# Performance work log

Hardware: AMD Instinct MI355X
Metric: run time of the kernel (lower is better)

The kernel has to match this reference:

```python
import jax, jax.numpy as jnp
import numpy as np

N_HEADS = 16
D_HEAD = 64
D_MODEL = 1024
WINDOW = 256
B, T = 4, 2048


def rotate_half(x):
    x1, x2 = jnp.split(x, 2, axis=-1)
    return jnp.concatenate([-x2, x1], axis=-1)


def apply_rope(x, cos, sin):
    return x * cos + rotate_half(x) * sin


def setup_inputs() -> dict:
    key = jax.random.key(0)
    ks = jax.random.split(key, 5)
    x = jax.random.normal(ks[0], (B, T, D_MODEL), dtype=jnp.float32)
    cos = jax.random.normal(ks[1], (1, T, 1, D_HEAD), dtype=jnp.float32)
    sin = jax.random.normal(ks[2], (1, T, 1, D_HEAD), dtype=jnp.float32)
    qkv_w = jax.random.normal(ks[3], (3 * D_MODEL, D_MODEL), dtype=jnp.float32) * (D_MODEL ** -0.5)
    out_w = jax.random.normal(ks[4], (D_MODEL, D_MODEL), dtype=jnp.float32) * (D_MODEL ** -0.5)
    return {"x": x, "cos": cos, "sin": sin, "qkv_w": qkv_w, "out_w": out_w}


def reference(x, cos, sin, qkv_w, out_w):
    Bc, Tc, C = x.shape
    # QKV projection (bias-free Linear: y = x @ W^T)
    qkv = jnp.einsum('btc,fc->btf', x, qkv_w)
    q, k, v = jnp.split(qkv, 3, axis=-1)
    # [B, H, T, d]
    def to_heads(t):
        return t.reshape(Bc, Tc, N_HEADS, D_HEAD).transpose(0, 2, 1, 3)
    q, k, v = to_heads(q), to_heads(k), to_heads(v)
    # RoPE: cos/sin [1, T, 1, d] -> [1, 1, T, d] broadcasting over heads
    cos_t = cos[:, :Tc].transpose(0, 2, 1, 3)
    sin_t = sin[:, :Tc].transpose(0, 2, 1, 3)
    q = apply_rope(q, cos_t, sin_t)
    k = apply_rope(k, cos_t, sin_t)
    # banded causal mask: allow j <= i and j >= i - (window-1)
    i = jnp.arange(Tc)[:, None]
    j = jnp.arange(Tc)[None, :]
    allowed = (j <= i) & (j >= i - (WINDOW - 1))  # [T, T]
    scale = 1.0 / jnp.sqrt(jnp.asarray(D_HEAD, dtype=q.dtype))
    scores = jnp.einsum('bhqd,bhkd->bhqk', q, k) * scale
    scores = jnp.where(allowed[None, None], scores, jnp.finfo(scores.dtype).min)
    attn = jax.nn.softmax(scores, axis=-1)
    out = jnp.einsum('bhqk,bhkd->bhqd', attn, v)
    out = out.transpose(0, 2, 1, 3).reshape(Bc, Tc, C)
    return jnp.einsum('btc,oc->bto', out, out_w)
```

## Files before the change

kernel.cpp:

```cpp
#include <hip/hip_runtime.h>

typedef __bf16 bf16_t;
typedef __bf16 bf16x8 __attribute__((ext_vector_type(8)));
typedef __bf16 bf16x4 __attribute__((ext_vector_type(4)));
typedef float f32x4 __attribute__((ext_vector_type(4)));

#define GLOAD_LDS16(gptr, lptr)                                                              \
  __builtin_amdgcn_global_load_lds((const __attribute__((address_space(1))) void*)(gptr),    \
                                   (__attribute__((address_space(3))) void*)(lptr), 16, 0, 0)

__device__ __forceinline__ f32x4 f32x4_zero() {
  f32x4 v; v[0] = 0.f; v[1] = 0.f; v[2] = 0.f; v[3] = 0.f; return v;
}

__device__ __forceinline__ int kxr(int r) { return (r & 7) ^ (((r >> 3) & 3) << 1); }

__global__ void cast3_kernel(const float* __restrict__ a, const float* __restrict__ b,
                             const float* __restrict__ c, bf16_t* __restrict__ oa,
                             bf16_t* __restrict__ ob, bf16_t* __restrict__ oc) {
  int i = blockIdx.x * blockDim.x + threadIdx.x;
  const float* src; bf16_t* dst; int j;
  if (i < 2097152) { src = a; dst = oa; j = i; }
  else if (i < 2883584) { src = b; dst = ob; j = i - 2097152; }
  else { src = c; dst = oc; j = i - 2883584; }
  float4 v = ((const float4*)src)[j];
  bf16x4 o;
  o[0] = (bf16_t)v.x; o[1] = (bf16_t)v.y; o[2] = (bf16_t)v.z; o[3] = (bf16_t)v.w;
  ((bf16x4*)dst)[j] = o;
}

#define GT_AELE 16384
#define GT_BELE 8192
#define GT_TILE (GT_AELE + GT_BELE)

__device__ __forceinline__ void gt_stage(const bf16_t* __restrict__ A,
                                         const bf16_t* __restrict__ B, bf16_t* buf,
                                         int bm, int bn, int t, int K, int tid) {
#pragma unroll
  for (int i = 0; i < 4; i++) {
    int gi = tid + i * 512;
    int row = gi >> 3, g = gi & 7;
    const bf16_t* src = A + (size_t)(bm * 256 + row) * K + t * 64 + ((g ^ (row & 7)) << 3);
    GLOAD_LDS16(src, buf + gi * 8);
  }
#pragma unroll
  for (int i = 0; i < 2; i++) {
    int gi = tid + i * 512;
    int row = gi >> 3, g = gi & 7;
    const bf16_t* src = B + (size_t)(bn * 128 + row) * K + t * 64 + ((g ^ (row & 7)) << 3);
    GLOAD_LDS16(src, buf + GT_AELE + gi * 8);
  }
}

template <int MODE>
__global__ __launch_bounds__(512, 1) void gemm_bt_kernel(
    const bf16_t* __restrict__ A, const bf16_t* __restrict__ B, float* __restrict__ C,
    bf16_t* __restrict__ oq, bf16_t* __restrict__ ok_, bf16_t* __restrict__ ov,
    const float* __restrict__ cosp, const float* __restrict__ sinp,
    int M, int N, int K) {
  __shared__ bf16_t lds[3 * GT_TILE];

  const int tid = threadIdx.x;
  const int lane = tid & 63;
  const int wid = tid >> 6;
  const int wr = wid >> 1;
  const int wc = wid & 1;
  const int l16 = lane & 15;
  const int qd = lane >> 4;
  const int bm = blockIdx.x, bn = blockIdx.y;

  f32x4 acc[4][4];
#pragma unroll
  for (int m = 0; m < 4; m++)
#pragma unroll
    for (int n = 0; n < 4; n++) acc[m][n] = f32x4_zero();

  const int NT = K >> 6;

  gt_stage(A, B, lds, bm, bn, 0, K, tid);
  gt_stage(A, B, lds + GT_TILE, bm, bn, 1, K, tid);
  asm volatile("s_waitcnt vmcnt(6)" ::: "memory");
  __builtin_amdgcn_s_barrier();
  __builtin_amdgcn_sched_barrier(0);

  int s = 0;
  for (int j = 0; j < NT; ++j) {
    if (j + 2 < NT) {
      int s2 = s + 2; if (s2 >= 3) s2 -= 3;
      gt_stage(A, B, lds + s2 * GT_TILE, bm, bn, j + 2, K, tid);
    }

    const bf16_t* bufc = lds + s * GT_TILE;
    bf16x8 af[4][2], bf[4][2];
#pragma unroll
    for (int m = 0; m < 4; m++)
#pragma unroll
      for (int kk = 0; kk < 2; kk++) {
        int row = wr * 64 + m * 16 + l16;
        af[m][kk] = *(const bf16x8*)&bufc[row * 64 + (((kk * 4 + qd) ^ (row & 7)) << 3)];
      }
#pragma unroll
    for (int n = 0; n < 4; n++)
#pragma unroll
      for (int kk = 0; kk < 2; kk++) {
        int row = wc * 64 + n * 16 + l16;
        bf[n][kk] = *(const bf16x8*)&bufc[GT_AELE + row * 64 + (((kk * 4 + qd) ^ (row & 7)) << 3)];
      }

    __builtin_amdgcn_s_setprio(1);
#pragma unroll
    for (int m = 0; m < 4; m++)
#pragma unroll
      for (int n = 0; n < 4; n++)
#pragma unroll
        for (int kk = 0; kk < 2; kk++)
          acc[m][n] = __builtin_amdgcn_mfma_f32_16x16x32_bf16(af[m][kk], bf[n][kk], acc[m][n], 0, 0, 0);
    __builtin_amdgcn_s_setprio(0);

    if (j + 2 < NT) {
      asm volatile("s_waitcnt vmcnt(6)" ::: "memory");
    } else {
      asm volatile("s_waitcnt vmcnt(0)" ::: "memory");
    }
    __builtin_amdgcn_s_barrier();
    __builtin_amdgcn_sched_barrier(0);
    s = (s == 2) ? 0 : s + 1;
  }

  if (MODE == 0) {
#pragma unroll
    for (int m = 0; m < 4; m++)
#pragma unroll
      for (int n = 0; n < 4; n++)
#pragma unroll
        for (int r = 0; r < 4; r++) {
          int row = bm * 256 + wr * 64 + m * 16 + qd * 4 + r;
          int col = bn * 128 + wc * 64 + n * 16 + l16;
          C[(size_t)row * N + col] = acc[m][n][r];
        }
  } else {
    const int colbase = bn * 128 + wc * 64;
    const int part = colbase >> 10;
    const int h = (colbase & 1023) >> 6;
    bf16_t* dst = (part == 0) ? oq : (part == 1) ? ok_ : ov;
    if (part == 2) {
#pragma unroll
      for (int m = 0; m < 4; m++)
#pragma unroll
        for (int r = 0; r < 4; r++) {
          int row = bm * 256 + wr * 64 + m * 16 + qd * 4 + r;
          int b = row >> 11, t = row & 2047;
          size_t basei = (((size_t)(b * 16 + h)) * 2048 + t) * 64;
#pragma unroll
          for (int n = 0; n < 4; n++)
            dst[basei + n * 16 + l16] = (bf16_t)acc[m][n][r];
        }
    } else {
      const float qsc = (part == 0) ? 0.18033688011112042f : 1.0f;
#pragma unroll
      for (int m = 0; m < 4; m++)
#pragma unroll
        for (int r = 0; r < 4; r++) {
          int row = bm * 256 + wr * 64 + m * 16 + qd * 4 + r;
          int b = row >> 11, t = row & 2047;
          size_t basei = (((size_t)(b * 16 + h)) * 2048 + t) * 64;
#pragma unroll
          for (int nb = 0; nb < 2; nb++) {
            int d = nb * 16 + l16;
            float xl = acc[m][nb][r];
            float xh = acc[m][nb + 2][r];
            float cl = cosp[t * 64 + d], ch = cosp[t * 64 + d + 32];
            float sl = sinp[t * 64 + d], sh = sinp[t * 64 + d + 32];
            dst[basei + d]      = (bf16_t)((xl * cl - xh * sl) * qsc);
            dst[basei + d + 32] = (bf16_t)((xh * ch + xl * sh) * qsc);
          }
        }
    }
  }
}

__global__ __launch_bounds__(256) void attn_kernel(
    const bf16_t* __restrict__ qh, const bf16_t* __restrict__ kh,
    const bf16_t* __restrict__ vh, bf16_t* __restrict__ ao) {
  __shared__ bf16_t qs[64 * 64];
  __shared__ bf16_t ks[64 * 64];
  __shared__ bf16_t vs[64 * 64];
  __shared__ bf16_t vswz[8 * 64 * 8];
  __shared__ bf16_t ps[4][16 * 64];

  const int tid = threadIdx.x;
  const int lane = tid & 63;
  const int wid = tid >> 6;
  const int l16 = lane & 15;
  const int qd = lane >> 4;

  const int bh = blockIdx.x;
  const int i0 = blockIdx.y * 64;
  const int b = bh >> 4, h = bh & 15;

  auto swz4 = [](int f) { int r = f >> 3; return r * 8 + ((f & 7) ^ (r & 7)); };
  const int r0 = tid >> 3, q0 = tid & 7;

  {
    const uint4* src = (const uint4*)(qh + ((size_t)bh * 2048 + i0) * 64);
    uint4* dst = (uint4*)qs;
    dst[swz4(tid)] = src[tid];
    dst[swz4(tid + 256)] = src[tid + 256];
  }

  bf16x8 bones;
#pragma unroll
  for (int e = 0; e < 8; e++) bones[e] = (bf16_t)1.0f;

  float l_i[4] = {0.f, 0.f, 0.f, 0.f};
  f32x4 oacc[4];
#pragma unroll
  for (int nb = 0; nb < 4; nb++) oacc[nb] = f32x4_zero();

  const int c1 = i0 >> 6;
  const int c0 = (c1 >= 4) ? (c1 - 4) : 0;

  for (int c = c0; c <= c1; c++) {
    const int j0 = c * 64;
    __syncthreads();
    {
      const uint4* ksrc = (const uint4*)(kh + ((size_t)bh * 2048 + j0) * 64);
      const uint4* vsrc = (const uint4*)(vh + ((size_t)bh * 2048 + j0) * 64);
      uint4* kdst = (uint4*)ks; uint4* vdst = (uint4*)vs;
      kdst[swz4(tid)] = ksrc[tid]; kdst[swz4(tid + 256)] = ksrc[tid + 256];
      vdst[r0 * 8 + (q0 ^ kxr(r0))] = vsrc[tid];
      vdst[(r0 + 32) * 8 + (q0 ^ kxr(r0 + 32))] = vsrc[tid + 256];
    }
    __syncthreads();

    f32x4 sacc[4];
#pragma unroll
    for (int nb = 0; nb < 4; nb++) sacc[nb] = f32x4_zero();
#pragma unroll
    for (int kk = 0; kk < 2; kk++) {
      bf16x8 afr = *(const bf16x8*)&qs[(wid * 16 + l16) * 64 + (((kk * 4 + qd) ^ (l16 & 7)) * 8)];
#pragma unroll
      for (int nb = 0; nb < 4; nb++) {
        bf16x8 bfr = *(const bf16x8*)&ks[(nb * 16 + l16) * 64 + (((kk * 4 + qd) ^ (l16 & 7)) * 8)];
        sacc[nb] = __builtin_amdgcn_mfma_f32_16x16x32_bf16(afr, bfr, sacc[nb], 0, 0, 0);
      }
    }

#pragma unroll
    for (int p2 = 0; p2 < 2; p2++) {
      int combo = p2 * 4 + wid;
      int jbase = (combo >> 2) * 32 + (lane >> 4) * 8;
      int dcol = (combo & 3) * 16 + (lane & 15);
      int bb = dcol >> 3, dlo = dcol & 7;
      bf16x8 v8;
#pragma unroll
      for (int e = 0; e < 8; e++) {
        int row = jbase + e;
        v8[e] = vs[row * 64 + ((bb ^ kxr(row)) * 8) + dlo];
      }
      *(bf16x8*)&vswz[(combo * 64 + lane) * 8] = v8;
    }

#pragma unroll
    for (int r = 0; r < 4; r++) {
      const int i = i0 + wid * 16 + qd * 4 + r;
      const int prow = qd * 4 + r;
#pragma unroll
      for (int nb = 0; nb < 4; nb++) {
        const int j = j0 + nb * 16 + l16;
        bool valid = (j <= i) && (j + 256 > i);
        float p = valid ? exp2f(sacc[nb][r]) : 0.f;
        ps[wid][prow * 64 + (((nb * 2 + (l16 >> 3)) ^ (prow & 7)) * 8) + (l16 & 7)] = (bf16_t)p;
      }
    }

    __syncthreads();

    f32x4 lacc = f32x4_zero();
#pragma unroll
    for (int kk = 0; kk < 2; kk++) {
      bf16x8 afr = *(const bf16x8*)&ps[wid][l16 * 64 + (((kk * 4 + qd) ^ (l16 & 7)) * 8)];
      lacc = __builtin_amdgcn_mfma_f32_16x16x32_bf16(afr, bones, lacc, 0, 0, 0);
#pragma unroll
      for (int nb = 0; nb < 4; nb++) {
        bf16x8 bfr = *(const bf16x8*)&vswz[((kk * 4 + nb) * 64 + lane) * 8];
        oacc[nb] = __builtin_amdgcn_mfma_f32_16x16x32_bf16(afr, bfr, oacc[nb], 0, 0, 0);
      }
    }
#pragma unroll
    for (int r = 0; r < 4; r++) l_i[r] += lacc[r];
  }

#pragma unroll
  for (int nb = 0; nb < 4; nb++) {
#pragma unroll
    for (int r = 0; r < 4; r++) {
      int t = i0 + wid * 16 + qd * 4 + r;
      ao[((size_t)(b * 2048 + t)) * 1024 + h * 64 + nb * 16 + l16] =
          (bf16_t)(oacc[nb][r] / l_i[r]);
    }
  }
}

extern "C" void kernel_launch(void* const* d_in, const int* in_sizes, int n_in,
                              void* d_out, int out_size, void* d_ws, size_t ws_size,
                              hipStream_t stream) {
  const float* x    = (const float*)d_in[0];
  const float* cosp = (const float*)d_in[1];
  const float* sinp = (const float*)d_in[2];
  const float* qkvw = (const float*)d_in[3];
  const float* outw = (const float*)d_in[4];
  float* out = (float*)d_out;

  char* ws = (char*)d_ws;
  bf16_t* xb  = (bf16_t*)(ws + 0);
  bf16_t* qwb = (bf16_t*)(ws + 16777216);
  bf16_t* owb = (bf16_t*)(ws + 23068672);
  bf16_t* qhp = (bf16_t*)(ws + 25165824);
  bf16_t* khp = (bf16_t*)(ws + 41943040);
  bf16_t* vhp = (bf16_t*)(ws + 58720256);
  bf16_t* aop = (bf16_t*)(ws + 75497472);

  cast3_kernel<<<12288, 256, 0, stream>>>(x, qkvw, outw, xb, qwb, owb);

  gemm_bt_kernel<1><<<dim3(32, 24), 512, 0, stream>>>(xb, qwb, nullptr, qhp, khp, vhp,
                                                      cosp, sinp, 8192, 3072, 1024);
  attn_kernel<<<dim3(64, 32), 256, 0, stream>>>(qhp, khp, vhp, aop);
  gemm_bt_kernel<0><<<dim3(32, 8), 512, 0, stream>>>(aop, owb, out, nullptr, nullptr, nullptr,
                                                     nullptr, nullptr, 8192, 1024, 1024);
}
```

Before: 219.0 us.

## Store V transposed from QKV GEMM epilogue and drop in-kernel V transpose

The QKV GEMM epilogue now writes V in a [B,H,d,T] transposed layout, staging each warp's tile through LDS so the global stores are 16-byte vectors. The attention kernel then loads V^T straight into a swizzled LDS tile that the PV MFMA can read directly. This removes the per-chunk scalar LDS gather into vswz and replaces one __syncthreads with a local lgkmcnt wait, since each warp reads only its own P rows. The risks are reusing the GEMM's LDS buffer in the epilogue and the uncoalesced 2048-stride rows of V^T loads.

```diff
diff --git a/kernel.cpp b/kernel.cpp
--- a/kernel.cpp
+++ b/kernel.cpp
@@ -12,8 +12,6 @@
 __device__ __forceinline__ f32x4 f32x4_zero() {
   f32x4 v; v[0] = 0.f; v[1] = 0.f; v[2] = 0.f; v[3] = 0.f; return v;
 }
-
-__device__ __forceinline__ int kxr(int r) { return (r & 7) ^ (((r >> 3) & 3) << 1); }
 
 __global__ void cast3_kernel(const float* __restrict__ a, const float* __restrict__ b,
                              const float* __restrict__ c, bf16_t* __restrict__ oa,
@@ -142,20 +140,35 @@
     const int colbase = bn * 128 + wc * 64;
     const int part = colbase >> 10;
     const int h = (colbase & 1023) >> 6;
-    bf16_t* dst = (part == 0) ? oq : (part == 1) ? ok_ : ov;
     if (part == 2) {
+      bf16_t* lw = lds + wid * 4096;
 #pragma unroll
       for (int m = 0; m < 4; m++)
 #pragma unroll
-        for (int r = 0; r < 4; r++) {
-          int row = bm * 256 + wr * 64 + m * 16 + qd * 4 + r;
-          int b = row >> 11, t = row & 2047;
-          size_t basei = (((size_t)(b * 16 + h)) * 2048 + t) * 64;
-#pragma unroll
-          for (int n = 0; n < 4; n++)
-            dst[basei + n * 16 + l16] = (bf16_t)acc[m][n][r];
+        for (int n = 0; n < 4; n++) {
+          int d = n * 16 + l16;
+          int gr = (m * 2 + (qd >> 1)) ^ (d & 7);
+          bf16x4 w;
+          w[0] = (bf16_t)acc[m][n][0];
+          w[1] = (bf16_t)acc[m][n][1];
+          w[2] = (bf16_t)acc[m][n][2];
+          w[3] = (bf16_t)acc[m][n][3];
+          *(bf16x4*)&lw[d * 64 + gr * 8 + (qd & 1) * 4] = w;
         }
+      asm volatile("s_waitcnt lgkmcnt(0)" ::: "memory");
+      __builtin_amdgcn_sched_barrier(0);
+      const int rowbase = bm * 256 + wr * 64;
+      const int bb = rowbase >> 11, tb = rowbase & 2047;
+      bf16_t* vbase = ov + ((size_t)(bb * 16 + h) * 64) * 2048 + tb;
+#pragma unroll
+      for (int it = 0; it < 8; it++) {
+        int d = it * 8 + (lane >> 3);
+        int g = lane & 7;
+        *(bf16x8*)&vbase[(size_t)d * 2048 + g * 8] =
+            *(const bf16x8*)&lw[d * 64 + ((g ^ (d & 7)) << 3)];
+      }
     } else {
+      bf16_t* dst = (part == 0) ? oq : ok_;
       const float qsc = (part == 0) ? 0.18033688011112042f : 1.0f;
 #pragma unroll
       for (int m = 0; m < 4; m++)
@@ -181,11 +194,10 @@
 
 __global__ __launch_bounds__(256) void attn_kernel(
     const bf16_t* __restrict__ qh, const bf16_t* __restrict__ kh,
-    const bf16_t* __restrict__ vh, bf16_t* __restrict__ ao) {
+    const bf16_t* __restrict__ vt, bf16_t* __restrict__ ao) {
   __shared__ bf16_t qs[64 * 64];
   __shared__ bf16_t ks[64 * 64];
-  __shared__ bf16_t vs[64 * 64];
-  __shared__ bf16_t vswz[8 * 64 * 8];
+  __shared__ bf16_t vts[64 * 64];
   __shared__ bf16_t ps[4][16 * 64];
 
   const int tid = threadIdx.x;
@@ -199,7 +211,6 @@
   const int b = bh >> 4, h = bh & 15;
 
   auto swz4 = [](int f) { int r = f >> 3; return r * 8 + ((f & 7) ^ (r & 7)); };
-  const int r0 = tid >> 3, q0 = tid & 7;
 
   {
     const uint4* src = (const uint4*)(qh + ((size_t)bh * 2048 + i0) * 64);
@@ -225,11 +236,16 @@
     __syncthreads();
     {
       const uint4* ksrc = (const uint4*)(kh + ((size_t)bh * 2048 + j0) * 64);
-      const uint4* vsrc = (const uint4*)(vh + ((size_t)bh * 2048 + j0) * 64);
-      uint4* kdst = (uint4*)ks; uint4* vdst = (uint4*)vs;
-      kdst[swz4(tid)] = ksrc[tid]; kdst[swz4(tid + 256)] = ksrc[tid + 256];
-      vdst[r0 * 8 + (q0 ^ kxr(r0))] = vsrc[tid];
-      vdst[(r0 + 32) * 8 + (q0 ^ kxr(r0 + 32))] = vsrc[tid + 256];
+      uint4* kdst = (uint4*)ks;
+      uint4* vdst = (uint4*)vts;
+      kdst[swz4(tid)] = ksrc[tid];
+      kdst[swz4(tid + 256)] = ksrc[tid + 256];
+      {
+        int f = tid;
+        vdst[swz4(f)] = *(const uint4*)(vt + (size_t)(bh * 64 + (f >> 3)) * 2048 + j0 + (f & 7) * 8);
+        f = tid + 256;
+        vdst[swz4(f)] = *(const uint4*)(vt + (size_t)(bh * 64 + (f >> 3)) * 2048 + j0 + (f & 7) * 8);
+      }
     }
     __syncthreads();
 
@@ -244,21 +260,6 @@
         bf16x8 bfr = *(const bf16x8*)&ks[(nb * 16 + l16) * 64 + (((kk * 4 + qd) ^ (l16 & 7)) * 8)];
         sacc[nb] = __builtin_amdgcn_mfma_f32_16x16x32_bf16(afr, bfr, sacc[nb], 0, 0, 0);
       }
-    }
-
-#pragma unroll
-    for (int p2 = 0; p2 < 2; p2++) {
-      int combo = p2 * 4 + wid;
-      int jbase = (combo >> 2) * 32 + (lane >> 4) * 8;
-      int dcol = (combo & 3) * 16 + (lane & 15);
-      int bb = dcol >> 3, dlo = dcol & 7;
-      bf16x8 v8;
-#pragma unroll
-      for (int e = 0; e < 8; e++) {
-        int row = jbase + e;
-        v8[e] = vs[row * 64 + ((bb ^ kxr(row)) * 8) + dlo];
-      }
-      *(bf16x8*)&vswz[(combo * 64 + lane) * 8] = v8;
     }
 
 #pragma unroll
@@ -274,7 +275,8 @@
       }
     }
 
-    __syncthreads();
+    asm volatile("s_waitcnt lgkmcnt(0)" ::: "memory");
+    __builtin_amdgcn_sched_barrier(0);
 
     f32x4 lacc = f32x4_zero();
 #pragma unroll
@@ -283,7 +285,7 @@
       lacc = __builtin_amdgcn_mfma_f32_16x16x32_bf16(afr, bones, lacc, 0, 0, 0);
 #pragma unroll
       for (int nb = 0; nb < 4; nb++) {
-        bf16x8 bfr = *(const bf16x8*)&vswz[((kk * 4 + nb) * 64 + lane) * 8];
+        bf16x8 bfr = *(const bf16x8*)&vts[(nb * 16 + l16) * 64 + (((kk * 4 + qd) ^ (l16 & 7)) * 8)];
         oacc[nb] = __builtin_amdgcn_mfma_f32_16x16x32_bf16(afr, bfr, oacc[nb], 0, 0, 0);
       }
     }
@@ -318,14 +320,14 @@
   bf16_t* owb = (bf16_t*)(ws + 23068672);
   bf16_t* qhp = (bf16_t*)(ws + 25165824);
   bf16_t* khp = (bf16_t*)(ws + 41943040);
-  bf16_t* vhp = (bf16_t*)(ws + 58720256);
+  bf16_t* vtp = (bf16_t*)(ws + 58720256);
   bf16_t* aop = (bf16_t*)(ws + 75497472);
 
   cast3_kernel<<<12288, 256, 0, stream>>>(x, qkvw, outw, xb, qwb, owb);
 
-  gemm_bt_kernel<1><<<dim3(32, 24), 512, 0, stream>>>(xb, qwb, nullptr, qhp, khp, vhp,
+  gemm_bt_kernel<1><<<dim3(32, 24), 512, 0, stream>>>(xb, qwb, nullptr, qhp, khp, vtp,
                                                       cosp, sinp, 8192, 3072, 1024);
-  attn_kernel<<<dim3(64, 32), 256, 0, stream>>>(qhp, khp, vhp, aop);
+  attn_kernel<<<dim3(64, 32), 256, 0, stream>>>(qhp, khp, vtp, aop);
   gemm_bt_kernel<0><<<dim3(32, 8), 512, 0, stream>>>(aop, owb, out, nullptr, nullptr, nullptr,
                                                      nullptr, nullptr, 8192, 1024, 1024);
 }
```

Result: faster. 214.2 us (-2.2%).
